# Optimization experiments

Measured on AMD Instinct MI355X. Metric: run time of the kernel, lower is better.

## Reference

```python
import jax, jax.numpy as jnp
import numpy as np

B, T, D_MODEL, D_HEAD = 8, 2048, 1024, 64


def setup_inputs() -> dict:
    key = jax.random.key(0)
    kx, kq, kk, kv = jax.random.split(key, 4)
    s = 1.0 / np.sqrt(D_MODEL)
    return {
        "x": jax.random.normal(kx, (B, T, D_MODEL), dtype=jnp.float32),
        "W_Q": jax.random.normal(kq, (D_MODEL, D_HEAD), dtype=jnp.float32) * s,
        "W_K": jax.random.normal(kk, (D_MODEL, D_HEAD), dtype=jnp.float32) * s,
        "W_V": jax.random.normal(kv, (D_MODEL, D_HEAD), dtype=jnp.float32) * s,
    }


def reference(x, W_Q, W_K, W_V):
    # x: [B, T, d_model]; projections -> [B, T, d_head]
    q = jnp.einsum("btd,dh->bth", x, W_Q)
    k = jnp.einsum("btd,dh->bth", x, W_K)
    v = jnp.einsum("btd,dh->bth", x, W_V)
    d_head = W_Q.shape[-1]
    scale = 1.0 / jnp.sqrt(jnp.asarray(d_head, dtype=x.dtype))
    # scores: [B, T, T], causal mask (lower-triangular kept)
    scores = jnp.einsum("bqh,bkh->bqk", q, k) * scale
    T_ = x.shape[1]
    causal = jnp.tril(jnp.ones((T_, T_), dtype=bool))
    scores = jnp.where(causal[None, :, :], scores, jnp.asarray(-jnp.inf, dtype=x.dtype))
    a = jax.nn.softmax(scores, axis=-1)
    # dropout omitted (eval mode / identity)
    out = jnp.einsum("bqk,bkh->bqh", a, v)
    return out
```

## Files before the change

### kernel.cpp

```cpp
#include <hip/hip_runtime.h>

#define TT   2048
#define DM   1024
#define DH   64
#define NB   8
#define BK   128
#define KST  72

typedef __attribute__((ext_vector_type(4))) float          f32x4;
typedef __attribute__((ext_vector_type(4))) int            i32x4;
typedef __attribute__((ext_vector_type(4))) unsigned short u16x4;
typedef __attribute__((ext_vector_type(8))) short          s16x8;

__device__ __forceinline__ unsigned short f2bf(float f) {
  unsigned int u = __float_as_uint(f);
  u += 0x7fffu + ((u >> 16) & 1u);
  return (unsigned short)(u >> 16);
}

#define MFMA(acc, a, b) \
  (acc) = __builtin_amdgcn_mfma_f32_16x16x32_bf16((a), (b), (acc), 0, 0, 0)

__device__ __forceinline__ void gload_lds16(const void* g, void* l) {
  __builtin_amdgcn_global_load_lds(
      (const __attribute__((address_space(1))) void*)g,
      (__attribute__((address_space(3))) void*)l, 16, 0, 0);
}

#define WS_WT    0u
#define WS_QK    393216u
#define WS_VT    4587520u
#define WS_OP    6684672u
#define WS_ML    24510464u

__global__ __launch_bounds__(256) void pack_w_kernel(
    const float* __restrict__ wq, const float* __restrict__ wk,
    const float* __restrict__ wv, unsigned short* __restrict__ wt) {
  int idx = blockIdx.x * 256 + threadIdx.x;
  if (idx >= 192 * DM) return;
  int n = idx >> 10;
  int k = idx & (DM - 1);
  const float* src = (n < 64) ? wq : ((n < 128) ? wk : wv);
  wt[(size_t)n * DM + k] = f2bf(src[(size_t)k * DH + (n & 63)]);
}

__global__ __launch_bounds__(256) void qkv_gemm_kernel(
    const float* __restrict__ x, const unsigned short* __restrict__ wt,
    unsigned short* __restrict__ qkvqk, unsigned short* __restrict__ vt) {
  __shared__ __align__(16) float          a_lds[32 * BK];
  __shared__ __align__(16) unsigned short b_lds[192 * BK];

  const int tid  = threadIdx.x;
  const int lane = tid & 63;
  const int w    = tid >> 6;
  const int ln   = lane & 15;
  const int quad = lane >> 4;
  const int mw   = w & 1;
  const int nw   = w >> 1;
  const int m0   = blockIdx.x * 32;
  const int n0   = nw * 96;
  const int lsw  = ln & 7;

  int agoff[4];
  #pragma unroll
  for (int i = 0; i < 4; ++i) {
    int s = i * 256 + w * 64 + lane;
    int m = s >> 5, cc = s & 31;
    agoff[i] = (m0 + m) * DM + ((cc ^ (m & 7)) << 2);
  }
  int bgoff[12];
  #pragma unroll
  for (int j = 0; j < 12; ++j) {
    int s = j * 256 + w * 64 + lane;
    int n = s >> 4, cc = s & 15;
    bgoff[j] = n * DM + ((cc ^ (n & 7)) << 3);
  }

  f32x4 acc[6];
  #pragma unroll
  for (int i = 0; i < 6; ++i) acc[i] = (f32x4){0.f, 0.f, 0.f, 0.f};
  union { s16x8 v; unsigned short h[8]; } ap;

  #pragma unroll
  for (int i = 0; i < 4; ++i)
    gload_lds16(x + agoff[i], (void*)(a_lds + (i * 256 + w * 64) * 4));
  #pragma unroll
  for (int j = 0; j < 12; ++j)
    gload_lds16(wt + bgoff[j], (void*)(b_lds + (j * 256 + w * 64) * 8));

  for (int k0 = 0; k0 < DM; k0 += BK) {
    __syncthreads();
    #pragma unroll
    for (int ks = 0; ks < BK; ks += 32) {
      const int m  = mw * 16 + ln;
      const int c0 = (ks >> 2) + 2 * quad;
      f32x4 v0 = *(const f32x4*)&a_lds[m * BK + ((c0 ^ lsw) << 2)];
      f32x4 v1 = *(const f32x4*)&a_lds[m * BK + (((c0 + 1) ^ lsw) << 2)];
      #pragma unroll
      for (int j = 0; j < 4; ++j) { ap.h[j] = f2bf(v0[j]); ap.h[4 + j] = f2bf(v1[j]); }
      s16x8 af = ap.v;
      const int cb = (ks >> 3) + quad;
      #pragma unroll
      for (int nt = 0; nt < 6; ++nt) {
        int n = n0 + nt * 16 + ln;
        s16x8 bf = *(const s16x8*)&b_lds[n * BK + ((cb ^ lsw) << 3)];
        MFMA(acc[nt], af, bf);
      }
    }
    __syncthreads();
    if (k0 + BK < DM) {
      const int kn = k0 + BK;
      #pragma unroll
      for (int i = 0; i < 4; ++i)
        gload_lds16(x + agoff[i] + kn, (void*)(a_lds + (i * 256 + w * 64) * 4));
      #pragma unroll
      for (int j = 0; j < 12; ++j)
        gload_lds16(wt + bgoff[j] + kn, (void*)(b_lds + (j * 256 + w * 64) * 8));
    }
  }

  const float QS = 0.18033688011112042f;
  const int mm0 = m0 + mw * 16;
  const int bz  = mm0 >> 11;
  const int tb  = (mm0 & 2047) + quad * 4;
  #pragma unroll
  for (int nt = 0; nt < 6; ++nt) {
    const int ncol = n0 + nt * 16 + ln;
    if (ncol < 128) {
      const float sc = (ncol < 64) ? QS : 1.0f;
      #pragma unroll
      for (int r = 0; r < 4; ++r) {
        int row = mm0 + quad * 4 + r;
        qkvqk[(size_t)row * 128 + ncol] = f2bf(acc[nt][r] * sc);
      }
    } else {
      int d = ncol - 128;
      u16x4 h;
      #pragma unroll
      for (int r = 0; r < 4; ++r) h[r] = f2bf(acc[nt][r]);
      *(u16x4*)(vt + ((size_t)bz * 64 + d) * TT + tb) = h;
    }
  }
}

__global__ __launch_bounds__(512) void attn_part_kernel(
    const unsigned short* __restrict__ qkvqk, const unsigned short* __restrict__ vt,
    unsigned short* __restrict__ opart, float* __restrict__ ml) {
  const int Ctab[16] = {0,1,3,6,10,15,21,28,36,45,55,66,78,91,105,120};
  const int f  = blockIdx.x;
  const int bz = f / 136;
  const int rw = f - bz * 136;
  int s = 0;
  #pragma unroll
  for (int t = 1; t < 16; ++t) if (rw >= Ctab[t]) s = t;
  const int c = rw - Ctab[s];

  __shared__ __align__(16) unsigned short k_lds[128 * 64];
  __shared__ __align__(16) unsigned short v_lds[64 * 128];
  __shared__ __align__(16) unsigned short p_lds[2 * 64 * KST];

  const int tid  = threadIdx.x;
  const int w    = tid >> 6;
  const int grp  = w >> 2;
  const int wq   = w & 3;
  const int lane = tid & 63;
  const int ln   = lane & 15;
  const int quad = lane >> 4;
  const int lsw  = ln & 7;
  const int bb   = bz * TT;
  const int kbase = c * 128;
  const int qt   = 2 * s + grp;

  #pragma unroll
  for (int i = 0; i < 2; ++i) {
    int base = i * 512 + w * 64;
    int slot = base + lane;
    int row = slot >> 3, cc = slot & 7;
    gload_lds16(qkvqk + (size_t)(bb + kbase + row) * 128 + 64 + ((cc ^ (row & 7)) << 3),
                (void*)(k_lds + base * 8));
  }
  #pragma unroll
  for (int i = 0; i < 2; ++i) {
    int base = i * 512 + w * 64;
    int slot = base + lane;
    int d = slot >> 4, cc = slot & 15;
    gload_lds16(vt + ((size_t)bz * 64 + d) * TT + kbase + ((cc ^ (d & 7)) << 3),
                (void*)(v_lds + base * 8));
  }

  const unsigned short* qrow = qkvqk + (size_t)(bb + qt * 64 + wq * 16 + ln) * 128;
  const s16x8 qf0 = *(const s16x8*)(qrow + quad * 8);
  const s16x8 qf1 = *(const s16x8*)(qrow + 32 + quad * 8);

  s16x8 ones;
  #pragma unroll
  for (int j = 0; j < 8; ++j) ones[j] = (short)0x3F80;

  f32x4 acc_o[4], acc_l;
  #pragma unroll
  for (int i = 0; i < 4; ++i) acc_o[i] = (f32x4){0.f, 0.f, 0.f, 0.f};
  acc_l = (f32x4){0.f, 0.f, 0.f, 0.f};

  unsigned short* pb = p_lds + grp * 64 * KST;
  const int qg = qt * 64 + wq * 16 + quad * 4;
  __syncthreads();

  #pragma unroll
  for (int ct = 0; ct < 2; ++ct) {
    const int ktg = c * 2 + ct;
    if (ktg <= qt) {
      const bool diag = (ktg == qt);
      f32x4 acc_s[4];
      #pragma unroll
      for (int i = 0; i < 4; ++i) acc_s[i] = (f32x4){0.f, 0.f, 0.f, 0.f};
      #pragma unroll
      for (int ns = 0; ns < 4; ++ns) {
        const int krow = ct * 64 + ns * 16 + ln;
        s16x8 kf0 = *(const s16x8*)&k_lds[krow * 64 + ((quad ^ lsw) << 3)];
        s16x8 kf1 = *(const s16x8*)&k_lds[krow * 64 + (((4 + quad) ^ lsw) << 3)];
        MFMA(acc_s[ns], qf0, kf0);
        MFMA(acc_s[ns], qf1, kf1);
      }
      #pragma unroll
      for (int r = 0; r < 4; ++r) {
        const int qgr = qg + r;
        #pragma unroll
        for (int ns = 0; ns < 4; ++ns) {
          float sv = acc_s[ns][r];
          if (diag) {
            int kg = ktg * 64 + ns * 16 + ln;
            sv = (kg <= qgr) ? sv : -1e30f;
          }
          pb[(wq * 16 + quad * 4 + r) * KST + ns * 16 + ln] =
              f2bf(__builtin_amdgcn_exp2f(sv));
        }
      }
      #pragma unroll
      for (int kk = 0; kk < 64; kk += 32) {
        s16x8 pf = *(const s16x8*)&pb[(wq * 16 + ln) * KST + kk + quad * 8];
        MFMA(acc_l, pf, ones);
        #pragma unroll
        for (int nt = 0; nt < 4; ++nt) {
          const int d  = nt * 16 + ln;
          const int sc = (ct * 8 + (kk >> 3) + quad) ^ lsw;
          s16x8 vf = *(const s16x8*)&v_lds[d * 128 + sc * 8];
          MFMA(acc_o[nt], pf, vf);
        }
      }
      asm volatile("" ::: "memory");
    }
  }

  const int base = (qt & 1) ? (s + 1) * (s + 1) : s * (s + 1);
  const size_t slab = (size_t)bz * 272 + base + c;
  unsigned short* op = opart + slab * 4096;
  #pragma unroll
  for (int nt = 0; nt < 4; ++nt)
    #pragma unroll
    for (int r = 0; r < 4; ++r)
      op[(wq * 16 + quad * 4 + r) * 64 + nt * 16 + ln] = f2bf(acc_o[nt][r]);
  if (ln == 0) {
    float* lp = ml + slab * 64;
    #pragma unroll
    for (int r = 0; r < 4; ++r)
      lp[wq * 16 + quad * 4 + r] = acc_l[r];
  }
}

__global__ __launch_bounds__(256) void attn_combine_kernel(
    const unsigned short* __restrict__ opart, const float* __restrict__ ml,
    float* __restrict__ out) {
  const int qt = blockIdx.x;
  const int bz = blockIdx.y;
  const int g  = qt >> 1;
  const int nch = g + 1;
  const int base = (qt & 1) ? (g + 1) * (g + 1) : g * (g + 1);
  const size_t slab0 = (size_t)bz * 272 + base;

  const int tid = threadIdx.x;
  const int row = tid >> 2;
  const int ds  = (tid & 3) * 16;

  float L = 0.f;
  float acc[16];
  #pragma unroll
  for (int j = 0; j < 16; ++j) acc[j] = 0.f;
  #pragma unroll 4
  for (int ch = 0; ch < nch; ++ch) {
    L += ml[(slab0 + ch) * 64 + row];
    const unsigned short* op = opart + (slab0 + ch) * 4096 + row * 64 + ds;
    i32x4 v0 = *(const i32x4*)(op);
    i32x4 v1 = *(const i32x4*)(op + 8);
    #pragma unroll
    for (int j = 0; j < 4; ++j) {
      unsigned int u0 = (unsigned int)v0[j], u1 = (unsigned int)v1[j];
      acc[j * 2]         += __uint_as_float(u0 << 16);
      acc[j * 2 + 1]     += __uint_as_float(u0 & 0xffff0000u);
      acc[8 + j * 2]     += __uint_as_float(u1 << 16);
      acc[8 + j * 2 + 1] += __uint_as_float(u1 & 0xffff0000u);
    }
  }
  float inv = 1.0f / L;
  float* o = out + ((size_t)bz * TT + qt * 64 + row) * 64 + ds;
  #pragma unroll
  for (int j = 0; j < 16; ++j) o[j] = acc[j] * inv;
}

extern "C" void kernel_launch(void* const* d_in, const int* in_sizes, int n_in,
                              void* d_out, int out_size, void* d_ws, size_t ws_size,
                              hipStream_t stream) {
  const float* x  = (const float*)d_in[0];
  const float* wq = (const float*)d_in[1];
  const float* wk = (const float*)d_in[2];
  const float* wv = (const float*)d_in[3];
  float* out = (float*)d_out;

  char* ws = (char*)d_ws;
  unsigned short* wt    = (unsigned short*)(ws + WS_WT);
  unsigned short* qkvqk = (unsigned short*)(ws + WS_QK);
  unsigned short* vt    = (unsigned short*)(ws + WS_VT);
  unsigned short* opart = (unsigned short*)(ws + WS_OP);
  float*          ml    = (float*)(ws + WS_ML);

  pack_w_kernel<<<(192 * DM + 255) / 256, 256, 0, stream>>>(wq, wk, wv, wt);
  qkv_gemm_kernel<<<NB * TT / 32, 256, 0, stream>>>(x, wt, qkvqk, vt);
  attn_part_kernel<<<NB * 136, 512, 0, stream>>>(qkvqk, vt, opart, ml);
  attn_combine_kernel<<<dim3(32, NB), 256, 0, stream>>>(opart, ml, out);
}
```

Baseline: 132.3 us.

## Loop key chunks inside attention blocks with double-buffered LDS and two-way split

The attention kernel now launches one block per (batch, query-tile pair, parity) instead of one block per (query-tile pair, 128-key chunk). Each block walks every second key chunk in a loop, prefetching the next K/V chunk into a second LDS buffer while it computes the current one. The combine step now sums only two partial outputs per query tile instead of up to sixteen, which cuts partial-output write and read traffic and shrinks the workspace. The cost is a grid of only 256 blocks with a causal load imbalance: the last query pair walks eight chunks while the first walks one. There is also less latency hiding from co-resident blocks.

```diff
diff --git a/kernel.cpp b/kernel.cpp
--- a/kernel.cpp
+++ b/kernel.cpp
@@ -31,7 +31,7 @@
 #define WS_QK    393216u
 #define WS_VT    4587520u
 #define WS_OP    6684672u
-#define WS_ML    24510464u
+#define WS_ML    10878976u
 
 __global__ __launch_bounds__(256) void pack_w_kernel(
     const float* __restrict__ wq, const float* __restrict__ wk,
@@ -146,17 +146,14 @@
 __global__ __launch_bounds__(512) void attn_part_kernel(
     const unsigned short* __restrict__ qkvqk, const unsigned short* __restrict__ vt,
     unsigned short* __restrict__ opart, float* __restrict__ ml) {
-  const int Ctab[16] = {0,1,3,6,10,15,21,28,36,45,55,66,78,91,105,120};
   const int f  = blockIdx.x;
-  const int bz = f / 136;
-  const int rw = f - bz * 136;
-  int s = 0;
-  #pragma unroll
-  for (int t = 1; t < 16; ++t) if (rw >= Ctab[t]) s = t;
-  const int c = rw - Ctab[s];
-
-  __shared__ __align__(16) unsigned short k_lds[128 * 64];
-  __shared__ __align__(16) unsigned short v_lds[64 * 128];
+  const int bz = f >> 5;
+  const int rr = f & 31;
+  const int s  = rr >> 1;
+  const int h  = rr & 1;
+
+  __shared__ __align__(16) unsigned short k_lds[2][128 * 64];
+  __shared__ __align__(16) unsigned short v_lds[2][64 * 128];
   __shared__ __align__(16) unsigned short p_lds[2 * 64 * KST];
 
   const int tid  = threadIdx.x;
@@ -168,25 +165,28 @@
   const int quad = lane >> 4;
   const int lsw  = ln & 7;
   const int bb   = bz * TT;
-  const int kbase = c * 128;
   const int qt   = 2 * s + grp;
 
-  #pragma unroll
-  for (int i = 0; i < 2; ++i) {
-    int base = i * 512 + w * 64;
-    int slot = base + lane;
-    int row = slot >> 3, cc = slot & 7;
-    gload_lds16(qkvqk + (size_t)(bb + kbase + row) * 128 + 64 + ((cc ^ (row & 7)) << 3),
-                (void*)(k_lds + base * 8));
-  }
-  #pragma unroll
-  for (int i = 0; i < 2; ++i) {
-    int base = i * 512 + w * 64;
-    int slot = base + lane;
-    int d = slot >> 4, cc = slot & 15;
-    gload_lds16(vt + ((size_t)bz * 64 + d) * TT + kbase + ((cc ^ (d & 7)) << 3),
-                (void*)(v_lds + base * 8));
-  }
+  auto stage = [&](int c, int buf) {
+    const int kbase = c * 128;
+    #pragma unroll
+    for (int i = 0; i < 2; ++i) {
+      int base = i * 512 + w * 64;
+      int slot = base + lane;
+      int row = slot >> 3, cc = slot & 7;
+      gload_lds16(
+          qkvqk + (size_t)(bb + kbase + row) * 128 + 64 + ((cc ^ (row & 7)) << 3),
+          (void*)(k_lds[buf] + base * 8));
+    }
+    #pragma unroll
+    for (int i = 0; i < 2; ++i) {
+      int base = i * 512 + w * 64;
+      int slot = base + lane;
+      int d = slot >> 4, cc = slot & 15;
+      gload_lds16(vt + ((size_t)bz * 64 + d) * TT + kbase + ((cc ^ (d & 7)) << 3),
+                  (void*)(v_lds[buf] + base * 8));
+    }
+  };
 
   const unsigned short* qrow = qkvqk + (size_t)(bb + qt * 64 + wq * 16 + ln) * 128;
   const s16x8 qf0 = *(const s16x8*)(qrow + quad * 8);
@@ -203,56 +203,65 @@
 
   unsigned short* pb = p_lds + grp * 64 * KST;
   const int qg = qt * 64 + wq * 16 + quad * 4;
-  __syncthreads();
-
-  #pragma unroll
-  for (int ct = 0; ct < 2; ++ct) {
-    const int ktg = c * 2 + ct;
-    if (ktg <= qt) {
-      const bool diag = (ktg == qt);
-      f32x4 acc_s[4];
-      #pragma unroll
-      for (int i = 0; i < 4; ++i) acc_s[i] = (f32x4){0.f, 0.f, 0.f, 0.f};
-      #pragma unroll
-      for (int ns = 0; ns < 4; ++ns) {
-        const int krow = ct * 64 + ns * 16 + ln;
-        s16x8 kf0 = *(const s16x8*)&k_lds[krow * 64 + ((quad ^ lsw) << 3)];
-        s16x8 kf1 = *(const s16x8*)&k_lds[krow * 64 + (((4 + quad) ^ lsw) << 3)];
-        MFMA(acc_s[ns], qf0, kf0);
-        MFMA(acc_s[ns], qf1, kf1);
-      }
-      #pragma unroll
-      for (int r = 0; r < 4; ++r) {
-        const int qgr = qg + r;
+
+  if (h <= s) stage(h, 0);
+
+  int it = 0;
+  for (int c = h; c <= s; c += 2, ++it) {
+    const int cur = it & 1;
+    __syncthreads();
+    if (c + 2 <= s) stage(c + 2, cur ^ 1);
+    const unsigned short* kb = k_lds[cur];
+    const unsigned short* vb = v_lds[cur];
+
+    #pragma unroll
+    for (int ct = 0; ct < 2; ++ct) {
+      const int ktg = c * 2 + ct;
+      if (ktg <= qt) {
+        const bool diag = (ktg == qt);
+        f32x4 acc_s[4];
+        #pragma unroll
+        for (int i = 0; i < 4; ++i) acc_s[i] = (f32x4){0.f, 0.f, 0.f, 0.f};
         #pragma unroll
         for (int ns = 0; ns < 4; ++ns) {
-          float sv = acc_s[ns][r];
-          if (diag) {
-            int kg = ktg * 64 + ns * 16 + ln;
-            sv = (kg <= qgr) ? sv : -1e30f;
+          const int krow = ct * 64 + ns * 16 + ln;
+          s16x8 kf0 = *(const s16x8*)&kb[krow * 64 + ((quad ^ lsw) << 3)];
+          s16x8 kf1 = *(const s16x8*)&kb[krow * 64 + (((4 + quad) ^ lsw) << 3)];
+          MFMA(acc_s[ns], qf0, kf0);
+          MFMA(acc_s[ns], qf1, kf1);
+        }
+        #pragma unroll
+        for (int r = 0; r < 4; ++r) {
+          const int qgr = qg + r;
+          #pragma unroll
+          for (int ns = 0; ns < 4; ++ns) {
+            float sv = acc_s[ns][r];
+            if (diag) {
+              int kg = ktg * 64 + ns * 16 + ln;
+              sv = (kg <= qgr) ? sv : -1e30f;
+            }
+            pb[(wq * 16 + quad * 4 + r) * KST + ns * 16 + ln] =
+                f2bf(__builtin_amdgcn_exp2f(sv));
           }
-          pb[(wq * 16 + quad * 4 + r) * KST + ns * 16 + ln] =
-              f2bf(__builtin_amdgcn_exp2f(sv));
         }
+        #pragma unroll
+        for (int kk = 0; kk < 64; kk += 32) {
+          s16x8 pf = *(const s16x8*)&pb[(wq * 16 + ln) * KST + kk + quad * 8];
+          MFMA(acc_l, pf, ones);
+          #pragma unroll
+          for (int nt = 0; nt < 4; ++nt) {
+            const int d  = nt * 16 + ln;
+            const int sc = (ct * 8 + (kk >> 3) + quad) ^ lsw;
+            s16x8 vf = *(const s16x8*)&vb[d * 128 + sc * 8];
+            MFMA(acc_o[nt], pf, vf);
+          }
+        }
+        asm volatile("" ::: "memory");
       }
-      #pragma unroll
-      for (int kk = 0; kk < 64; kk += 32) {
-        s16x8 pf = *(const s16x8*)&pb[(wq * 16 + ln) * KST + kk + quad * 8];
-        MFMA(acc_l, pf, ones);
-        #pragma unroll
-        for (int nt = 0; nt < 4; ++nt) {
-          const int d  = nt * 16 + ln;
-          const int sc = (ct * 8 + (kk >> 3) + quad) ^ lsw;
-          s16x8 vf = *(const s16x8*)&v_lds[d * 128 + sc * 8];
-          MFMA(acc_o[nt], pf, vf);
-        }
-      }
-      asm volatile("" ::: "memory");
-    }
-  }
-
-  const int base = (qt & 1) ? (s + 1) * (s + 1) : s * (s + 1);
-  const size_t slab = (size_t)bz * 272 + base + c;
+    }
+  }
+
+  const size_t slab = ((size_t)bz * 32 + qt) * 2 + h;
   unsigned short* op = opart + slab * 4096;
   #pragma unroll
   for (int nt = 0; nt < 4; ++nt)
@@ -272,10 +281,7 @@
     float* __restrict__ out) {
   const int qt = blockIdx.x;
   const int bz = blockIdx.y;
-  const int g  = qt >> 1;
-  const int nch = g + 1;
-  const int base = (qt & 1) ? (g + 1) * (g + 1) : g * (g + 1);
-  const size_t slab0 = (size_t)bz * 272 + base;
+  const size_t slab0 = ((size_t)bz * 32 + qt) * 2;
 
   const int tid = threadIdx.x;
   const int row = tid >> 2;
@@ -285,8 +291,8 @@
   float acc[16];
   #pragma unroll
   for (int j = 0; j < 16; ++j) acc[j] = 0.f;
-  #pragma unroll 4
-  for (int ch = 0; ch < nch; ++ch) {
+  #pragma unroll
+  for (int ch = 0; ch < 2; ++ch) {
     L += ml[(slab0 + ch) * 64 + row];
     const unsigned short* op = opart + (slab0 + ch) * 4096 + row * 64 + ds;
     i32x4 v0 = *(const i32x4*)(op);
@@ -324,6 +330,6 @@
 
   pack_w_kernel<<<(192 * DM + 255) / 256, 256, 0, stream>>>(wq, wk, wv, wt);
   qkv_gemm_kernel<<<NB * TT / 32, 256, 0, stream>>>(x, wt, qkvqk, vt);
-  attn_part_kernel<<<NB * 136, 512, 0, stream>>>(qkvqk, vt, opart, ml);
+  attn_part_kernel<<<NB * 32, 512, 0, stream>>>(qkvqk, vt, opart, ml);
   attn_combine_kernel<<<dim3(32, NB), 256, 0, stream>>>(opart, ml, out);
 }
```

Result: no change. 133.6 us (+1.0%).

## Split K/V tile loads into two halves to overlap second load with compute

Applied to the files above, without the earlier changes.

The 128-key K and V tile is now staged as two 64-key halves in separate LDS buffers. The first half is loaded and synchronized before compute starts. The second half's global-to-LDS loads are issued right after that barrier, so they run while the first sub-tile is being computed. A barrier after the first iteration makes the second half visible before it is used. This hides part of the load latency at the cost of an extra block-wide barrier, and blocks that skip the second tile still pay for its load.

```diff
diff --git a/kernel.cpp b/kernel.cpp
--- a/kernel.cpp
+++ b/kernel.cpp
@@ -155,8 +155,8 @@
   for (int t = 1; t < 16; ++t) if (rw >= Ctab[t]) s = t;
   const int c = rw - Ctab[s];
 
-  __shared__ __align__(16) unsigned short k_lds[128 * 64];
-  __shared__ __align__(16) unsigned short v_lds[64 * 128];
+  __shared__ __align__(16) unsigned short k_lds[2][64 * 64];
+  __shared__ __align__(16) unsigned short v_lds[2][64 * 64];
   __shared__ __align__(16) unsigned short p_lds[2 * 64 * KST];
 
   const int tid  = threadIdx.x;
@@ -171,22 +171,12 @@
   const int kbase = c * 128;
   const int qt   = 2 * s + grp;
 
-  #pragma unroll
-  for (int i = 0; i < 2; ++i) {
-    int base = i * 512 + w * 64;
-    int slot = base + lane;
-    int row = slot >> 3, cc = slot & 7;
-    gload_lds16(qkvqk + (size_t)(bb + kbase + row) * 128 + 64 + ((cc ^ (row & 7)) << 3),
-                (void*)(k_lds + base * 8));
-  }
-  #pragma unroll
-  for (int i = 0; i < 2; ++i) {
-    int base = i * 512 + w * 64;
-    int slot = base + lane;
-    int d = slot >> 4, cc = slot & 15;
-    gload_lds16(vt + ((size_t)bz * 64 + d) * TT + kbase + ((cc ^ (d & 7)) << 3),
-                (void*)(v_lds + base * 8));
-  }
+  const int slot = w * 64 + lane;
+  const int srow = slot >> 3, scc = slot & 7;
+  const unsigned short* kgp =
+      qkvqk + (size_t)(bb + kbase + srow) * 128 + 64 + ((scc ^ (srow & 7)) << 3);
+  const unsigned short* vgp =
+      vt + ((size_t)bz * 64 + srow) * TT + kbase + ((scc ^ (srow & 7)) << 3);
 
   const unsigned short* qrow = qkvqk + (size_t)(bb + qt * 64 + wq * 16 + ln) * 128;
   const s16x8 qf0 = *(const s16x8*)(qrow + quad * 8);
@@ -203,10 +193,17 @@
 
   unsigned short* pb = p_lds + grp * 64 * KST;
   const int qg = qt * 64 + wq * 16 + quad * 4;
+
+  gload_lds16(kgp, (void*)(k_lds[0] + (w * 64) * 8));
+  gload_lds16(vgp, (void*)(v_lds[0] + (w * 64) * 8));
   __syncthreads();
+  gload_lds16(kgp + 64 * 128, (void*)(k_lds[1] + (w * 64) * 8));
+  gload_lds16(vgp + 64,       (void*)(v_lds[1] + (w * 64) * 8));
 
   #pragma unroll
   for (int ct = 0; ct < 2; ++ct) {
+    const unsigned short* kb = k_lds[ct];
+    const unsigned short* vb = v_lds[ct];
     const int ktg = c * 2 + ct;
     if (ktg <= qt) {
       const bool diag = (ktg == qt);
@@ -215,9 +212,9 @@
       for (int i = 0; i < 4; ++i) acc_s[i] = (f32x4){0.f, 0.f, 0.f, 0.f};
       #pragma unroll
       for (int ns = 0; ns < 4; ++ns) {
-        const int krow = ct * 64 + ns * 16 + ln;
-        s16x8 kf0 = *(const s16x8*)&k_lds[krow * 64 + ((quad ^ lsw) << 3)];
-        s16x8 kf1 = *(const s16x8*)&k_lds[krow * 64 + (((4 + quad) ^ lsw) << 3)];
+        const int krow = ns * 16 + ln;
+        s16x8 kf0 = *(const s16x8*)&kb[krow * 64 + ((quad ^ lsw) << 3)];
+        s16x8 kf1 = *(const s16x8*)&kb[krow * 64 + (((4 + quad) ^ lsw) << 3)];
         MFMA(acc_s[ns], qf0, kf0);
         MFMA(acc_s[ns], qf1, kf1);
       }
@@ -242,13 +239,14 @@
         #pragma unroll
         for (int nt = 0; nt < 4; ++nt) {
           const int d  = nt * 16 + ln;
-          const int sc = (ct * 8 + (kk >> 3) + quad) ^ lsw;
-          s16x8 vf = *(const s16x8*)&v_lds[d * 128 + sc * 8];
+          const int sc = ((kk >> 3) + quad) ^ lsw;
+          s16x8 vf = *(const s16x8*)&vb[d * 64 + sc * 8];
           MFMA(acc_o[nt], pf, vf);
         }
       }
       asm volatile("" ::: "memory");
     }
+    if (ct == 0) __syncthreads();
   }
 
   const int base = (qt & 1) ? (s + 1) * (s + 1) : s * (s + 1);
```

After: 131.3 us. About the same (-0.8%).
